# Kernel optimization log

Hardware: AMD Instinct MI355X
Metric: run time of the kernel (lower is better)

Reference implementation:

```python
import jax, jax.numpy as jnp
import numpy as np

EPS = 1e-8  # torch cosine_similarity eps


def setup_inputs() -> dict:
    key = jax.random.key(0)
    k1, k2, k3 = jax.random.split(key, 3)
    N, D, n_classes = 512, 512, 10
    prediction = jax.random.normal(k1, (N, D), dtype=jnp.float32)
    # raw (pre-softplus) learnable distances, n_classes - 1 of them
    distances_raw = jax.random.uniform(k2, (n_classes - 1,), dtype=jnp.float32)
    target = jax.random.randint(k3, (N,), 0, n_classes)
    return {"prediction": prediction, "distances_raw": distances_raw, "target": target}


def reference(prediction, distances_raw, target):
    N = prediction.shape[0]
    # cosine similarity matrix [N, N]
    norms = jnp.linalg.norm(prediction, axis=1, keepdims=True)
    xn = prediction / jnp.maximum(norms, EPS)
    cos = xn @ xn.T

    same = target[:, None] == target[None, :]
    eye = jnp.eye(N, dtype=bool)
    positives = same & ~eye          # same-class pairs, excluding self
    negatives = ~same                # different-class pairs (diag excluded since same)

    # ordinal class positions on a line; pairwise class-center distances
    pos_d = jax.nn.softplus(distances_raw)
    class_pos = jnp.concatenate([jnp.zeros((1,), cos.dtype), jnp.cumsum(pos_d)])
    dist_matrix = jnp.abs(class_pos[:, None] - class_pos[None, :])
    margins = dist_matrix[target[:, None], target[None, :]]
    margins = jnp.where(negatives, margins, 0.0)

    # term[i, j, k] = relu(cos[i,j] + margin[i,j] - cos[i,k]),
    # valid only when (i,j) is a negative pair and (i,k) is a positive pair.
    term = jax.nn.relu((cos + margins)[:, :, None] - cos[:, None, :])  # [i,j,k]
    term = term * negatives[:, :, None].astype(cos.dtype) * positives[:, None, :].astype(cos.dtype)

    S = term.sum(axis=1)                                  # [i, k]
    n_neg = negatives.sum(axis=1).astype(cos.dtype)       # [i]
    count = positives.astype(cos.dtype) * n_neg[:, None]  # [i, k] valid-pair counts
    loss_ik = S / jnp.maximum(count, 1.0)

    # aggregate over positive anchors k, then mean over samples i
    tot = (loss_ik * (count > 0)).sum(axis=1) / jnp.maximum(count.sum(axis=1), 1.0)
    return tot.mean()
```

## Files before the change

kernel.cpp:

```cpp
#include <hip/hip_runtime.h>
#include <math.h>

#define N 512
#define D 512
#define NC 10
#define NSLICE 16
#define KS 32
#define MP 132
#define EPSF 1e-8f

__global__ __launch_bounds__(256) void k_gram(
    const float* __restrict__ pred,
    float* __restrict__ Gp,
    float* __restrict__ norm2) {
  __shared__ __align__(16) float As[KS][MP];
  __shared__ __align__(16) float Bs[KS][MP];

  const int bj = blockIdx.x, bi = blockIdx.y, s = blockIdx.z;
  const int t = threadIdx.x;
  const int tx = t & 15, ty = t >> 4;

#pragma unroll
  for (int j = 0; j < 4; j++) {
    int f = t + 256 * j;
    int r = f >> 3;
    int q = f & 7;
    float4 va = *(const float4*)(pred + (size_t)(bi * 128 + r) * D + s * KS + q * 4);
    float4 vb = *(const float4*)(pred + (size_t)(bj * 128 + r) * D + s * KS + q * 4);
    As[q * 4 + 0][r] = va.x; As[q * 4 + 1][r] = va.y;
    As[q * 4 + 2][r] = va.z; As[q * 4 + 3][r] = va.w;
    Bs[q * 4 + 0][r] = vb.x; Bs[q * 4 + 1][r] = vb.y;
    Bs[q * 4 + 2][r] = vb.z; Bs[q * 4 + 3][r] = vb.w;
  }
  __syncthreads();

  float acc[8][8];
#pragma unroll
  for (int r = 0; r < 8; r++)
#pragma unroll
    for (int c = 0; c < 8; c++) acc[r][c] = 0.0f;

#pragma unroll 4
  for (int k = 0; k < KS; k++) {
    float4 a0 = *(const float4*)(&As[k][ty * 8]);
    float4 a1 = *(const float4*)(&As[k][ty * 8 + 4]);
    float4 b0 = *(const float4*)(&Bs[k][tx * 8]);
    float4 b1 = *(const float4*)(&Bs[k][tx * 8 + 4]);
    float a[8] = {a0.x, a0.y, a0.z, a0.w, a1.x, a1.y, a1.z, a1.w};
    float b[8] = {b0.x, b0.y, b0.z, b0.w, b1.x, b1.y, b1.z, b1.w};
#pragma unroll
    for (int r = 0; r < 8; r++)
#pragma unroll
      for (int c = 0; c < 8; c++) acc[r][c] += a[r] * b[c];
  }

  float* Gs = Gp + (size_t)s * N * N;
  const int n0 = bj * 128 + tx * 8;
#pragma unroll
  for (int r = 0; r < 8; r++) {
    int m = bi * 128 + ty * 8 + r;
    float4 lo = {acc[r][0], acc[r][1], acc[r][2], acc[r][3]};
    float4 hi = {acc[r][4], acc[r][5], acc[r][6], acc[r][7]};
    *(float4*)(&Gs[(size_t)m * N + n0]) = lo;
    *(float4*)(&Gs[(size_t)m * N + n0 + 4]) = hi;
  }
  if (bi == bj && tx == ty) {
#pragma unroll
    for (int r = 0; r < 8; r++)
      atomicAdd(&norm2[bi * 128 + ty * 8 + r], acc[r][r]);
  }
}

__global__ __launch_bounds__(256) void k_rows(
    const float* __restrict__ Gp,
    const int* __restrict__ target,
    const float* __restrict__ norm2,
    const float* __restrict__ dist_raw,
    float* __restrict__ out) {
  const int i = blockIdx.x;
  const int tid = threadIdx.x;

  __shared__ float s_a[N];
  __shared__ float s_p[N];
  __shared__ float s_cp[NC];
  __shared__ int s_np, s_nn;

  if (tid == 0) {
    s_np = 0; s_nn = 0;
    float acc = 0.0f;
    s_cp[0] = 0.0f;
    for (int c = 0; c < NC - 1; c++) {
      acc += log1pf(expf(dist_raw[c]));
      s_cp[c + 1] = acc;
    }
  }
  __syncthreads();

  const int ti = target[i];
  const float inv_i = 1.0f / fmaxf(sqrtf(norm2[i]), EPSF);
  const float cpi = s_cp[ti];

  for (int j = tid; j < N; j += 256) {
    float g = 0.0f;
#pragma unroll
    for (int s = 0; s < NSLICE; s++)
      g += Gp[(size_t)s * N * N + (size_t)i * N + j];
    float cosv = g * inv_i * (1.0f / fmaxf(sqrtf(norm2[j]), EPSF));
    int tj = target[j];
    if (tj != ti) {
      float m = fabsf(cpi - s_cp[tj]);
      int idx = atomicAdd(&s_nn, 1);
      s_a[idx] = cosv + m;
    } else if (j != i) {
      int idx = atomicAdd(&s_np, 1);
      s_p[idx] = cosv;
    }
  }
  __syncthreads();

  const int np = s_np, nn = s_nn;
  float a0 = (tid < nn) ? s_a[tid] : -1e30f;
  float a1 = (tid + 256 < nn) ? s_a[tid + 256] : -1e30f;
  float acc = 0.0f;
  for (int kk = 0; kk < np; kk++) {
    float ck = s_p[kk];
    acc += fmaxf(a0 - ck, 0.0f) + fmaxf(a1 - ck, 0.0f);
  }

  for (int off = 32; off > 0; off >>= 1) acc += __shfl_down(acc, off);
  __shared__ float s_part[4];
  if ((tid & 63) == 0) s_part[tid >> 6] = acc;
  __syncthreads();
  if (tid == 0) {
    float total = s_part[0] + s_part[1] + s_part[2] + s_part[3];
    if (np > 0 && nn > 0) {
      float r = total / ((float)nn * (float)nn * (float)np);
      atomicAdd(out, r / (float)N);
    }
  }
}

extern "C" void kernel_launch(void* const* d_in, const int* in_sizes, int n_in,
                              void* d_out, int out_size, void* d_ws, size_t ws_size,
                              hipStream_t stream) {
  const float* pred = (const float*)d_in[0];
  const float* dist_raw = (const float*)d_in[1];
  const int* target = (const int*)d_in[2];
  float* out = (float*)d_out;

  float* Gp = (float*)d_ws;
  float* norm2 = Gp + (size_t)NSLICE * N * N;

  hipMemsetAsync(norm2, 0, N * sizeof(float), stream);
  hipMemsetAsync(out, 0, sizeof(float), stream);

  dim3 ggrid(4, 4, NSLICE);
  k_gram<<<ggrid, 256, 0, stream>>>(pred, Gp, norm2);
  k_rows<<<N, 256, 0, stream>>>(Gp, target, norm2, dist_raw, out);
}
```

Baseline: 88.68 us.

## Fuse Gram computation and row loss into one kernel, two rows per block

```diff
diff --git a/kernel.cpp b/kernel.cpp
--- a/kernel.cpp
+++ b/kernel.cpp
@@ -4,140 +4,121 @@
 #define N 512
 #define D 512
 #define NC 10
-#define NSLICE 16
-#define KS 32
-#define MP 132
 #define EPSF 1e-8f
 
-__global__ __launch_bounds__(256) void k_gram(
+__global__ __launch_bounds__(256) void k_fused(
     const float* __restrict__ pred,
-    float* __restrict__ Gp,
-    float* __restrict__ norm2) {
-  __shared__ __align__(16) float As[KS][MP];
-  __shared__ __align__(16) float Bs[KS][MP];
+    const float* __restrict__ dist_raw,
+    const int* __restrict__ target,
+    float* __restrict__ out) {
+  const int b = blockIdx.x;
+  const int t = threadIdx.x;
+  const int i0 = 2 * b, i1 = 2 * b + 1;
 
-  const int bj = blockIdx.x, bi = blockIdx.y, s = blockIdx.z;
-  const int t = threadIdx.x;
-  const int tx = t & 15, ty = t >> 4;
-
-#pragma unroll
-  for (int j = 0; j < 4; j++) {
-    int f = t + 256 * j;
-    int r = f >> 3;
-    int q = f & 7;
-    float4 va = *(const float4*)(pred + (size_t)(bi * 128 + r) * D + s * KS + q * 4);
-    float4 vb = *(const float4*)(pred + (size_t)(bj * 128 + r) * D + s * KS + q * 4);
-    As[q * 4 + 0][r] = va.x; As[q * 4 + 1][r] = va.y;
-    As[q * 4 + 2][r] = va.z; As[q * 4 + 3][r] = va.w;
-    Bs[q * 4 + 0][r] = vb.x; Bs[q * 4 + 1][r] = vb.y;
-    Bs[q * 4 + 2][r] = vb.z; Bs[q * 4 + 3][r] = vb.w;
-  }
-  __syncthreads();
-
-  float acc[8][8];
-#pragma unroll
-  for (int r = 0; r < 8; r++)
-#pragma unroll
-    for (int c = 0; c < 8; c++) acc[r][c] = 0.0f;
-
-#pragma unroll 4
-  for (int k = 0; k < KS; k++) {
-    float4 a0 = *(const float4*)(&As[k][ty * 8]);
-    float4 a1 = *(const float4*)(&As[k][ty * 8 + 4]);
-    float4 b0 = *(const float4*)(&Bs[k][tx * 8]);
-    float4 b1 = *(const float4*)(&Bs[k][tx * 8 + 4]);
-    float a[8] = {a0.x, a0.y, a0.z, a0.w, a1.x, a1.y, a1.z, a1.w};
-    float b[8] = {b0.x, b0.y, b0.z, b0.w, b1.x, b1.y, b1.z, b1.w};
-#pragma unroll
-    for (int r = 0; r < 8; r++)
-#pragma unroll
-      for (int c = 0; c < 8; c++) acc[r][c] += a[r] * b[c];
-  }
-
-  float* Gs = Gp + (size_t)s * N * N;
-  const int n0 = bj * 128 + tx * 8;
-#pragma unroll
-  for (int r = 0; r < 8; r++) {
-    int m = bi * 128 + ty * 8 + r;
-    float4 lo = {acc[r][0], acc[r][1], acc[r][2], acc[r][3]};
-    float4 hi = {acc[r][4], acc[r][5], acc[r][6], acc[r][7]};
-    *(float4*)(&Gs[(size_t)m * N + n0]) = lo;
-    *(float4*)(&Gs[(size_t)m * N + n0 + 4]) = hi;
-  }
-  if (bi == bj && tx == ty) {
-#pragma unroll
-    for (int r = 0; r < 8; r++)
-      atomicAdd(&norm2[bi * 128 + ty * 8 + r], acc[r][r]);
-  }
-}
-
-__global__ __launch_bounds__(256) void k_rows(
-    const float* __restrict__ Gp,
-    const int* __restrict__ target,
-    const float* __restrict__ norm2,
-    const float* __restrict__ dist_raw,
-    float* __restrict__ out) {
-  const int i = blockIdx.x;
-  const int tid = threadIdx.x;
-
-  __shared__ float s_a[N];
+  __shared__ __align__(16) float s_x0[D];
+  __shared__ __align__(16) float s_x1[D];
+  __shared__ float s_c0[N];
+  __shared__ float s_c1[N];
+  __shared__ int   s_t[N];
   __shared__ float s_p[N];
   __shared__ float s_cp[NC];
-  __shared__ int s_np, s_nn;
+  __shared__ float s_inv0, s_inv1;
+  __shared__ float s_part[4];
+  __shared__ int s_np;
 
-  if (tid == 0) {
-    s_np = 0; s_nn = 0;
-    float acc = 0.0f;
+  {
+    int which = t >> 7, q = t & 127;
+    float4 v = *(const float4*)(pred + (size_t)(i0 + which) * D + q * 4);
+    if (which == 0) *(float4*)(&s_x0[q * 4]) = v;
+    else            *(float4*)(&s_x1[q * 4]) = v;
+  }
+  s_t[t] = target[t];
+  s_t[t + 256] = target[t + 256];
+  if (t == 0) {
+    float a = 0.0f;
     s_cp[0] = 0.0f;
     for (int c = 0; c < NC - 1; c++) {
-      acc += log1pf(expf(dist_raw[c]));
-      s_cp[c + 1] = acc;
+      a += log1pf(expf(dist_raw[c]));
+      s_cp[c + 1] = a;
     }
   }
   __syncthreads();
 
-  const int ti = target[i];
-  const float inv_i = 1.0f / fmaxf(sqrtf(norm2[i]), EPSF);
-  const float cpi = s_cp[ti];
-
-  for (int j = tid; j < N; j += 256) {
-    float g = 0.0f;
+  for (int jj = 0; jj < 2; jj++) {
+    const int j = t + jj * 256;
+    const float4* rj = (const float4*)(pred + (size_t)j * D);
+    float4 a00 = {0, 0, 0, 0}, a01 = {0, 0, 0, 0}, ann = {0, 0, 0, 0};
+    float4 buf[8], nbuf[8];
 #pragma unroll
-    for (int s = 0; s < NSLICE; s++)
-      g += Gp[(size_t)s * N * N + (size_t)i * N + j];
-    float cosv = g * inv_i * (1.0f / fmaxf(sqrtf(norm2[j]), EPSF));
-    int tj = target[j];
-    if (tj != ti) {
-      float m = fabsf(cpi - s_cp[tj]);
-      int idx = atomicAdd(&s_nn, 1);
-      s_a[idx] = cosv + m;
-    } else if (j != i) {
-      int idx = atomicAdd(&s_np, 1);
-      s_p[idx] = cosv;
+    for (int u = 0; u < 8; u++) buf[u] = rj[u];
+    for (int g = 0; g < 16; g++) {
+      if (g < 15) {
+#pragma unroll
+        for (int u = 0; u < 8; u++) nbuf[u] = rj[(g + 1) * 8 + u];
+      }
+#pragma unroll
+      for (int u = 0; u < 8; u++) {
+        const int k4 = (g * 8 + u) * 4;
+        float4 v = buf[u];
+        float4 x0 = *(const float4*)(&s_x0[k4]);
+        float4 x1 = *(const float4*)(&s_x1[k4]);
+        a00.x += v.x * x0.x; a00.y += v.y * x0.y;
+        a00.z += v.z * x0.z; a00.w += v.w * x0.w;
+        a01.x += v.x * x1.x; a01.y += v.y * x1.y;
+        a01.z += v.z * x1.z; a01.w += v.w * x1.w;
+        ann.x += v.x * v.x;  ann.y += v.y * v.y;
+        ann.z += v.z * v.z;  ann.w += v.w * v.w;
+      }
+#pragma unroll
+      for (int u = 0; u < 8; u++) buf[u] = nbuf[u];
     }
+    float d00 = (a00.x + a00.y) + (a00.z + a00.w);
+    float d01 = (a01.x + a01.y) + (a01.z + a01.w);
+    float dnn = (ann.x + ann.y) + (ann.z + ann.w);
+    float invj = 1.0f / fmaxf(sqrtf(dnn), EPSF);
+    s_c0[j] = d00 * invj;
+    s_c1[j] = d01 * invj;
+    if (j == i0) s_inv0 = invj;
+    if (j == i1) s_inv1 = invj;
   }
   __syncthreads();
 
-  const int np = s_np, nn = s_nn;
-  float a0 = (tid < nn) ? s_a[tid] : -1e30f;
-  float a1 = (tid + 256 < nn) ? s_a[tid + 256] : -1e30f;
-  float acc = 0.0f;
-  for (int kk = 0; kk < np; kk++) {
-    float ck = s_p[kk];
-    acc += fmaxf(a0 - ck, 0.0f) + fmaxf(a1 - ck, 0.0f);
-  }
-
-  for (int off = 32; off > 0; off >>= 1) acc += __shfl_down(acc, off);
-  __shared__ float s_part[4];
-  if ((tid & 63) == 0) s_part[tid >> 6] = acc;
-  __syncthreads();
-  if (tid == 0) {
-    float total = s_part[0] + s_part[1] + s_part[2] + s_part[3];
-    if (np > 0 && nn > 0) {
-      float r = total / ((float)nn * (float)nn * (float)np);
-      atomicAdd(out, r / (float)N);
+  float contrib = 0.0f;
+#pragma unroll
+  for (int rr = 0; rr < 2; rr++) {
+    const int i = (rr == 0) ? i0 : i1;
+    const float inv_i = (rr == 0) ? s_inv0 : s_inv1;
+    const float* s_c = (rr == 0) ? s_c0 : s_c1;
+    const int ti = s_t[i];
+    const float cpi = s_cp[ti];
+    if (t == 0) s_np = 0;
+    __syncthreads();
+    const int j0 = t, j1 = t + 256;
+    const float c0 = s_c[j0] * inv_i;
+    const float c1 = s_c[j1] * inv_i;
+    const int t0v = s_t[j0], t1v = s_t[j1];
+    const bool p0 = (t0v == ti), p1 = (t1v == ti);
+    const float a0 = p0 ? -1e30f : (c0 + fabsf(cpi - s_cp[t0v]));
+    const float a1 = p1 ? -1e30f : (c1 + fabsf(cpi - s_cp[t1v]));
+    if (p0 && j0 != i) { int k = atomicAdd(&s_np, 1); s_p[k] = c0; }
+    if (p1 && j1 != i) { int k = atomicAdd(&s_np, 1); s_p[k] = c1; }
+    __syncthreads();
+    const int np = s_np;
+    const int nn = N - np - 1;
+    float acc = 0.0f;
+    for (int kk = 0; kk < np; kk++) {
+      float ck = s_p[kk];
+      acc += fmaxf(a0 - ck, 0.0f) + fmaxf(a1 - ck, 0.0f);
+    }
+    for (int off = 32; off > 0; off >>= 1) acc += __shfl_down(acc, off);
+    if ((t & 63) == 0) s_part[t >> 6] = acc;
+    __syncthreads();
+    if (t == 0 && np > 0 && nn > 0) {
+      float tot = s_part[0] + s_part[1] + s_part[2] + s_part[3];
+      contrib += tot / ((float)nn * (float)nn * (float)np) * (1.0f / (float)N);
     }
   }
+  if (t == 0) atomicAdd(out, contrib);
 }
 
 extern "C" void kernel_launch(void* const* d_in, const int* in_sizes, int n_in,
@@ -148,13 +129,6 @@
   const int* target = (const int*)d_in[2];
   float* out = (float*)d_out;
 
-  float* Gp = (float*)d_ws;
-  float* norm2 = Gp + (size_t)NSLICE * N * N;
-
-  hipMemsetAsync(norm2, 0, N * sizeof(float), stream);
   hipMemsetAsync(out, 0, sizeof(float), stream);
-
-  dim3 ggrid(4, 4, NSLICE);
-  k_gram<<<ggrid, 256, 0, stream>>>(pred, Gp, norm2);
-  k_rows<<<N, 256, 0, stream>>>(Gp, target, norm2, dist_raw, out);
+  k_fused<<<256, 256, 0, stream>>>(pred, dist_raw, target, out);
 }
```

After: 95.05 us. +7.2%, slower.
